# Kernel optimization log

Measured on AMD Instinct MI355X. Metric: run time of the kernel, lower is better.

Reference implementation:

```python
import jax, jax.numpy as jnp
import numpy as np

B, T, H, K = 4, 1024, 1024, 16
HD = H // K  # head dim
EPS = 1e-5


def _layernorm(x, g, b):
    mu = jnp.mean(x, axis=-1, keepdims=True)
    var = jnp.mean(jnp.square(x - mu), axis=-1, keepdims=True)
    return (x - mu) * jax.lax.rsqrt(var + EPS) * g + b


def setup_inputs() -> dict:
    key = jax.random.key(0)
    ks = jax.random.split(key, 16)
    s = 0.02
    return {
        "x": jax.random.normal(ks[0], (B, T, H), jnp.float32),
        "ln1_g": jnp.ones((H,), jnp.float32),
        "ln1_b": jnp.zeros((H,), jnp.float32),
        "ln2_g": jnp.ones((H,), jnp.float32),
        "ln2_b": jnp.zeros((H,), jnp.float32),
        "Wq": jax.random.normal(ks[1], (H, H), jnp.float32) * s,
        "bq": jnp.zeros((H,), jnp.float32),
        "Wk": jax.random.normal(ks[2], (H, H), jnp.float32) * s,
        "bk": jnp.zeros((H,), jnp.float32),
        "Wv": jax.random.normal(ks[3], (H, H), jnp.float32) * s,
        "bv": jnp.zeros((H,), jnp.float32),
        "W1": jax.random.normal(ks[4], (H, 4 * H), jnp.float32) * s,
        "b1": jnp.zeros((4 * H,), jnp.float32),
        "W2": jax.random.normal(ks[5], (4 * H, H), jnp.float32) * s,
        "b2": jnp.zeros((H,), jnp.float32),
    }


def reference(x, ln1_g, ln1_b, ln2_g, ln2_b, Wq, bq, Wk, bk, Wv, bv, W1, b1, W2, b2):
    # --- attention sub-block ---
    h = _layernorm(x, ln1_g, ln1_b)                      # (B,T,H)
    q = (h @ Wq + bq).reshape(B, T, K, HD).transpose(0, 2, 1, 3)  # (B,K,T,hd)
    k = (h @ Wk + bk).reshape(B, T, K, HD).transpose(0, 2, 1, 3)
    v = (h @ Wv + bv).reshape(B, T, K, HD).transpose(0, 2, 1, 3)
    qkt = jnp.einsum('bkqd,bkpd->bkqp', q, k)            # (B,K,T,T)
    attn = qkt * (1.0 / np.sqrt(HD))
    # module quirk: masked positions are FILLED with 1e-9 (not -inf) before softmax
    causal_mask = jnp.triu(jnp.ones((T, T), bool), k=1)  # True above diagonal = masked
    attn = jnp.where(causal_mask, jnp.float32(1e-9), attn)
    attn = jax.nn.softmax(attn, axis=-1)
    y = jnp.einsum('bkqp,bkpd->bkqd', attn, v)           # (B,K,T,hd)
    y = y.transpose(0, 2, 1, 3).reshape(B, T, H)
    x = x + y
    # --- MLP sub-block (dropout is identity at eval) ---
    h2 = _layernorm(x, ln2_g, ln2_b)
    m = jax.nn.gelu(h2 @ W1 + b1, approximate=False) @ W2 + b2
    return x + m
```

## Files before the change

### kernel.cpp

```cpp
#include <hip/hip_runtime.h>
#include <hip/hip_bf16.h>
#include <math.h>


typedef __attribute__((ext_vector_type(8))) short bf16x8;
typedef __attribute__((ext_vector_type(4))) float f32x4;

#define DEVINL __device__ __forceinline__

#define LOG2E_SCALE 0.18033688f
#define MASK2 1.4426950408889634e-9f

DEVINL void stage16(const __hip_bfloat16* g, short* l) {
  __builtin_amdgcn_global_load_lds(
      (const __attribute__((address_space(1))) unsigned int*)g,
      (__attribute__((address_space(3))) unsigned int*)l, 16, 0, 0);
}

DEVINL float bf2f(short u) {
  unsigned x = ((unsigned)(unsigned short)u) << 16;
  float f; __builtin_memcpy(&f, &x, 4); return f;
}

DEVINL short f2bf_s(float f) {
  __hip_bfloat16 h = __float2bfloat16(f);
  short s; __builtin_memcpy(&s, &h, 2); return s;
}

DEVINL float block_sum(float v, float* sb) {
  #pragma unroll
  for (int o = 32; o; o >>= 1) v += __shfl_down(v, o);
  const int lane = threadIdx.x & 63, w = threadIdx.x >> 6;
  if (lane == 0) sb[w] = v;
  __syncthreads();
  float r = sb[0] + sb[1] + sb[2] + sb[3];
  __syncthreads();
  return r;
}

template<int BM, int BN, int WM, int WN>
DEVINL void gemm_core64(const __hip_bfloat16* __restrict__ A, int lda,
                        const __hip_bfloat16* __restrict__ Bt, int ldb,
                        int Kd, int row0, int col0,
                        f32x4 (&acc)[WM/16][WN/16],
                        short* lds_a, short* lds_b) {
  constexpr int MI = WM / 16, NI = WN / 16, WNC = BN / WN;
  constexpr int CA = BM * 8, CB = BN * 8;
  const int tid = threadIdx.x;
  const int lane = tid & 63, wave = tid >> 6;
  const int wm = (wave / WNC) * WM, wn = (wave % WNC) * WN;
  const int lr = lane & 15, lq = lane >> 4;
  for (int k0 = 0; k0 < Kd; k0 += 64) {
    #pragma unroll
    for (int c = tid; c < CA; c += 256) {
      const int r = c >> 3, kc = ((c & 7) ^ (r & 7)) << 3;
      stage16(A + (size_t)(row0 + r) * lda + k0 + kc, lds_a + c * 8);
    }
    #pragma unroll
    for (int c = tid; c < CB; c += 256) {
      const int r = c >> 3, kc = ((c & 7) ^ (r & 7)) << 3;
      stage16(Bt + (size_t)(col0 + r) * ldb + k0 + kc, lds_b + c * 8);
    }
    __syncthreads();
    #pragma unroll
    for (int s = 0; s < 2; s++) {
      bf16x8 af[MI], bfr[NI];
      #pragma unroll
      for (int mi = 0; mi < MI; mi++) {
        const int m = wm + mi * 16 + lr;
        af[mi] = *(const bf16x8*)(lds_a + m * 64 + (((s * 4 + lq) ^ (m & 7)) << 3));
      }
      #pragma unroll
      for (int ni = 0; ni < NI; ni++) {
        const int n = wn + ni * 16 + lr;
        bfr[ni] = *(const bf16x8*)(lds_b + n * 64 + (((s * 4 + lq) ^ (n & 7)) << 3));
      }
      #pragma unroll
      for (int mi = 0; mi < MI; mi++)
        #pragma unroll
        for (int ni = 0; ni < NI; ni++)
          acc[mi][ni] = __builtin_amdgcn_mfma_f32_16x16x32_bf16(
              af[mi], bfr[ni], acc[mi][ni], 0, 0, 0);
    }
    __syncthreads();
  }
}

__global__ __launch_bounds__(256) void k_tcvt(const float* __restrict__ src,
                                              __hip_bfloat16* __restrict__ dst,
                                              int R, int C, int dstOff, int dstPitch) {
  __shared__ float tile[32][33];
  const int c0 = blockIdx.x * 32, r0 = blockIdx.y * 32;
  const int tx = threadIdx.x, ty = threadIdx.y;
  #pragma unroll
  for (int i = 0; i < 32; i += 8)
    tile[ty + i][tx] = src[(size_t)(r0 + ty + i) * C + c0 + tx];
  __syncthreads();
  #pragma unroll
  for (int i = 0; i < 32; i += 8)
    dst[(size_t)(c0 + ty + i + dstOff) * dstPitch + r0 + tx] =
        __float2bfloat16(tile[tx][ty + i]);
}

__global__ __launch_bounds__(256) void k_tcvt3(const float* __restrict__ Wq,
                                               const float* __restrict__ Wk,
                                               const float* __restrict__ Wv,
                                               __hip_bfloat16* __restrict__ dst) {
  __shared__ float tile[32][33];
  const float* src = blockIdx.z == 0 ? Wq : (blockIdx.z == 1 ? Wk : Wv);
  const int dstOff = blockIdx.z << 10;
  const int c0 = blockIdx.x * 32, r0 = blockIdx.y * 32;
  const int tx = threadIdx.x, ty = threadIdx.y;
  #pragma unroll
  for (int i = 0; i < 32; i += 8)
    tile[ty + i][tx] = src[(size_t)(r0 + ty + i) * 1024 + c0 + tx];
  __syncthreads();
  #pragma unroll
  for (int i = 0; i < 32; i += 8)
    dst[(size_t)(c0 + ty + i + dstOff) * 1024 + r0 + tx] =
        __float2bfloat16(tile[tx][ty + i]);
}

__global__ __launch_bounds__(256) void k_pack_bias(const float* __restrict__ bq,
                                                   const float* __restrict__ bk,
                                                   const float* __restrict__ bv,
                                                   float* __restrict__ o) {
  const int i = blockIdx.x * 256 + threadIdx.x;
  if (i < 3072)
    o[i] = i < 1024 ? bq[i] : (i < 2048 ? bk[i - 1024] : bv[i - 2048]);
}

__global__ __launch_bounds__(256) void k_ln(const float* __restrict__ x,
                                            const float* __restrict__ y,
                                            const float* __restrict__ g,
                                            const float* __restrict__ bb,
                                            __hip_bfloat16* __restrict__ o,
                                            const float* __restrict__ badd,
                                            float* __restrict__ oinit) {
  __shared__ float sb[4];
  const int t = threadIdx.x;
  const size_t base = (size_t)blockIdx.x * 1024 + t * 4;
  const int c = t * 4;
  float4 xv = *(const float4*)(x + base);
  if (y) {
    float4 yv = *(const float4*)(y + base);
    xv.x += yv.x; xv.y += yv.y; xv.z += yv.z; xv.w += yv.w;
    float4 ov;
    ov.x = xv.x + badd[c + 0]; ov.y = xv.y + badd[c + 1];
    ov.z = xv.z + badd[c + 2]; ov.w = xv.w + badd[c + 3];
    *(float4*)(oinit + base) = ov;
  }
  const float mu = block_sum(xv.x + xv.y + xv.z + xv.w, sb) * (1.f / 1024.f);
  const float dx = xv.x - mu, dy = xv.y - mu, dz = xv.z - mu, dw = xv.w - mu;
  const float var = block_sum(dx * dx + dy * dy + dz * dz + dw * dw, sb) * (1.f / 1024.f);
  const float rs = rsqrtf(var + 1e-5f);
  o[base + 0] = __float2bfloat16(dx * rs * g[c + 0] + bb[c + 0]);
  o[base + 1] = __float2bfloat16(dy * rs * g[c + 1] + bb[c + 1]);
  o[base + 2] = __float2bfloat16(dz * rs * g[c + 2] + bb[c + 2]);
  o[base + 3] = __float2bfloat16(dw * rs * g[c + 3] + bb[c + 3]);
}

__global__ __launch_bounds__(256) void k_gemm_qkv(
    const __hip_bfloat16* __restrict__ h1, const __hip_bfloat16* __restrict__ Wt,
    const float* __restrict__ bqkv, __hip_bfloat16* __restrict__ Q,
    __hip_bfloat16* __restrict__ K, __hip_bfloat16* __restrict__ Vt) {
  __shared__ alignas(16) short smem[16896];
  short* la = smem;
  short* lb = smem + 8192;
  short* lc = smem;
  const int row0 = blockIdx.x * 128, col0 = blockIdx.y * 128;
  f32x4 acc[4][4] = {};
  gemm_core64<128, 128, 64, 64>(h1, 1024, Wt, 1024, 1024, row0, col0, acc, la, lb);
  const int tid = threadIdx.x, lane = tid & 63, wave = tid >> 6;
  const int wm = (wave >> 1) * 64, wn = (wave & 1) * 64, lr = lane & 15, lq = lane >> 4;
  const int which = col0 >> 10;
  const int h0 = (col0 & 1023) >> 6;
  const int b = row0 >> 10, t0 = row0 & 1023;
  if (which < 2) {
    const float qs = (which == 0) ? LOG2E_SCALE : 1.f;
    #pragma unroll
    for (int mi = 0; mi < 4; mi++)
      #pragma unroll
      for (int ni = 0; ni < 4; ni++)
        #pragma unroll
        for (int r = 0; r < 4; r++) {
          const int row = wm + mi * 16 + lq * 4 + r;
          const int col = wn + ni * 16 + lr;
          lc[row * 132 + col] = f2bf_s((acc[mi][ni][r] + bqkv[col0 + col]) * qs);
        }
    __syncthreads();
    __hip_bfloat16* O = which == 0 ? Q : K;
    #pragma unroll
    for (int c = 0; c < 8; c++) {
      const int f = tid + 256 * c;
      const int r = f >> 4, cc = f & 15;
      const int col = cc * 8;
      const int head = h0 + (col >> 6), d = col & 63;
      float4 vv = *(const float4*)(lc + r * 132 + col);
      *(float4*)(O + (((size_t)(b * 16 + head)) << 16) + (t0 + r) * 64 + d) = vv;
    }
  } else {
    #pragma unroll
    for (int mi = 0; mi < 4; mi++)
      #pragma unroll
      for (int ni = 0; ni < 4; ni++)
        #pragma unroll
        for (int r = 0; r < 4; r++) {
          const int row = wm + mi * 16 + lq * 4 + r;
          const int col = wn + ni * 16 + lr;
          lc[col * 132 + row] = f2bf_s(acc[mi][ni][r] + bqkv[col0 + col]);
        }
    __syncthreads();
    #pragma unroll
    for (int c = 0; c < 8; c++) {
      const int f = tid + 256 * c;
      const int dl = f >> 4, tc = f & 15;
      const int head = h0 + (dl >> 6), d = dl & 63;
      float4 vv = *(const float4*)(lc + dl * 132 + tc * 8);
      *(float4*)(Vt + (((size_t)(b * 16 + head)) << 16) + (size_t)d * 1024 +
                 t0 + tc * 8) = vv;
    }
  }
}

__global__ __launch_bounds__(256) void k_tailv(const __hip_bfloat16* __restrict__ Vt,
                                               float* __restrict__ TV) {
  __shared__ float ts[8][64];
  const int hb = blockIdx.x, tid = threadIdx.x;
  const __hip_bfloat16* Vh = Vt + ((size_t)hb << 16);
  for (int w = tid; w < 512; w += 256) {
    const int kt = w >> 6, d = w & 63;
    const short* p = (const short*)(Vh + (size_t)d * 1024 + kt * 128);
    float s = 0.f;
    for (int j = 0; j < 128; j += 8) {
      bf16x8 v = *(const bf16x8*)(p + j);
      #pragma unroll
      for (int e = 0; e < 8; e++) s += bf2f(v[e]);
    }
    ts[kt][d] = s;
  }
  __syncthreads();
  for (int w = tid; w < 512; w += 256) {
    const int qt = w >> 6, d = w & 63;
    float s = 0.f;
    for (int kt = qt + 1; kt < 8; kt++) s += ts[kt][d];
    TV[((size_t)hb * 8 + qt) * 64 + d] = s;
  }
}

__global__ __launch_bounds__(256, 3) void k_attn(
    const __hip_bfloat16* __restrict__ Q, const __hip_bfloat16* __restrict__ K,
    const __hip_bfloat16* __restrict__ Vt, const float* __restrict__ TV,
    float* __restrict__ y) {
  __shared__ short lp[64 * 130];
  __shared__ short lK[128 * 64];
  __shared__ short lV[128 * 64];
  const int hb = blockIdx.y;
  const int j = (blockIdx.y & 32) ? (15 - (int)blockIdx.x) : (int)blockIdx.x;
  const int q0 = j * 64;
  const int nkt = (j >> 1) + 1;
  const int tid = threadIdx.x, lane = tid & 63, wave = tid >> 6;
  const int lr = lane & 15, lq = lane >> 4;
  const int wm = wave * 16;
  const __hip_bfloat16* Qh = Q + ((size_t)hb << 16);
  const __hip_bfloat16* Kh = K + ((size_t)hb << 16);
  const __hip_bfloat16* Vh = Vt + ((size_t)hb << 16);

  bf16x8 qf[2];
  #pragma unroll
  for (int s = 0; s < 2; s++)
    qf[s] = *(const bf16x8*)((const short*)Qh +
                             (size_t)(q0 + wm + lr) * 64 + s * 32 + lq * 8);

  f32x4 oacc[4] = {};
  float mrow[4], lrow[4];
  #pragma unroll
  for (int r = 0; r < 4; r++) { mrow[r] = -1e30f; lrow[r] = 0.f; }

  for (int c = tid; c < 1024; c += 256)
    stage16(Kh + (size_t)(c >> 3) * 64 + (((c & 7) ^ ((c >> 3) & 7)) << 3),
            lK + c * 8);
  __syncthreads();

  for (int kt = 0; kt < nkt; kt++) {
    const int k0 = kt * 128;
    f32x4 sacc[8] = {};
    __builtin_amdgcn_s_setprio(1);
    #pragma unroll
    for (int s = 0; s < 2; s++) {
      bf16x8 bf[8];
      #pragma unroll
      for (int ni = 0; ni < 8; ni++) {
        const int n = ni * 16 + lr;
        bf[ni] = *(const bf16x8*)(lK + n * 64 + (((s * 4 + lq) ^ (n & 7)) << 3));
      }
      #pragma unroll
      for (int ni = 0; ni < 8; ni++)
        sacc[ni] = __builtin_amdgcn_mfma_f32_16x16x32_bf16(
            qf[s], bf[ni], sacc[ni], 0, 0, 0);
    }
    __builtin_amdgcn_s_setprio(0);
    __syncthreads();
    for (int c = tid; c < 1024; c += 256)
      stage16(Vh + (size_t)(c >> 4) * 1024 + k0 + (((c & 15) ^ ((c >> 4) & 15)) << 3),
              lV + c * 8);
    if (kt + 1 < nkt) {
      const int k1 = k0 + 128;
      for (int c = tid; c < 1024; c += 256)
        stage16(Kh + (size_t)(k1 + (c >> 3)) * 64 + (((c & 7) ^ ((c >> 3) & 7)) << 3),
                lK + c * 8);
    }
    const bool last = (kt == nkt - 1);
    #pragma unroll
    for (int r = 0; r < 4; r++) {
      const int grow = q0 + wm + lq * 4 + r;
      float tmax = -1e30f;
      #pragma unroll
      for (int ni = 0; ni < 8; ni++) {
        float v = sacc[ni][r];
        if (last && (k0 + ni * 16 + lr) > grow) v = MASK2;
        sacc[ni][r] = v;
        tmax = fmaxf(tmax, v);
      }
      #pragma unroll
      for (int msk = 8; msk; msk >>= 1) tmax = fmaxf(tmax, __shfl_xor(tmax, msk));
      const float mn = fmaxf(mrow[r], tmax);
      const float al = __builtin_amdgcn_exp2f(mrow[r] - mn);
      float rs = 0.f;
      #pragma unroll
      for (int ni = 0; ni < 8; ni++) {
        const float pv = __builtin_amdgcn_exp2f(sacc[ni][r] - mn);
        sacc[ni][r] = pv;
        rs += pv;
      }
      #pragma unroll
      for (int msk = 8; msk; msk >>= 1) rs += __shfl_xor(rs, msk);
      mrow[r] = mn;
      lrow[r] = lrow[r] * al + rs;
      #pragma unroll
      for (int ni = 0; ni < 4; ni++) oacc[ni][r] *= al;
    }
    #pragma unroll
    for (int r = 0; r < 4; r++) {
      const int row = wm + lq * 4 + r;
      #pragma unroll
      for (int ni = 0; ni < 8; ni++)
        lp[row * 130 + ni * 16 + lr] = f2bf_s(sacc[ni][r]);
    }
    __syncthreads();
    __builtin_amdgcn_s_setprio(1);
    #pragma unroll
    for (int ks = 0; ks < 4; ks++) {
      bf16x8 pa, vb[4];
      pa = *(const bf16x8*)(lp + (wm + lr) * 130 + ks * 32 + lq * 8);
      #pragma unroll
      for (int ni = 0; ni < 4; ni++) {
        const int d = ni * 16 + lr;
        vb[ni] = *(const bf16x8*)(lV + d * 128 + (((ks * 4 + lq) ^ (d & 15)) << 3));
      }
      #pragma unroll
      for (int ni = 0; ni < 4; ni++)
        oacc[ni] = __builtin_amdgcn_mfma_f32_16x16x32_bf16(
            pa, vb[ni], oacc[ni], 0, 0, 0);
    }
    __builtin_amdgcn_s_setprio(0);
  }

  const int b = hb >> 4, h = hb & 15;
  const float cv = (float)(1024 - nkt * 128);
  const float* tv = TV + ((size_t)hb * 8 + (j >> 1)) * 64;
  #pragma unroll
  for (int r = 0; r < 4; r++) {
    const int t = q0 + wm + lq * 4 + r;
    const float tail = __builtin_amdgcn_exp2f(MASK2 - mrow[r]);
    const float inv = 1.f / (lrow[r] + cv * tail);
    #pragma unroll
    for (int ni = 0; ni < 4; ni++) {
      const int d = ni * 16 + lr;
      y[((size_t)(b * 1024 + t) << 10) + h * 64 + d] =
          (oacc[ni][r] + tail * tv[d]) * inv;
    }
  }
}

__global__ __launch_bounds__(256) void k_gemm_mlp1(const __hip_bfloat16* __restrict__ h2,
                                                   const __hip_bfloat16* __restrict__ W1t,
                                                   const float* __restrict__ b1,
                                                   __hip_bfloat16* __restrict__ G) {
  __shared__ alignas(16) short smem[16896];
  short* la = smem;
  short* lb = smem + 8192;
  short* lc = smem;
  const int row0 = blockIdx.x * 128, col0 = blockIdx.y * 128;
  f32x4 acc[4][4] = {};
  gemm_core64<128, 128, 64, 64>(h2, 1024, W1t, 1024, 1024, row0, col0, acc, la, lb);
  const int tid = threadIdx.x, lane = tid & 63, wave = tid >> 6;
  const int wm = (wave >> 1) * 64, wn = (wave & 1) * 64, lr = lane & 15, lq = lane >> 4;
  #pragma unroll
  for (int mi = 0; mi < 4; mi++)
    #pragma unroll
    for (int ni = 0; ni < 4; ni++)
      #pragma unroll
      for (int r = 0; r < 4; r++) {
        const int row = wm + mi * 16 + lq * 4 + r;
        const int col = wn + ni * 16 + lr;
        float v = acc[mi][ni][r] + b1[col0 + col];
        const float u = fminf(v * (2.3022079f + 0.1029434f * v * v), 80.f);
        const float e = __builtin_amdgcn_exp2f(u);
        v = v * e * __builtin_amdgcn_rcpf(e + 1.f);
        lc[row * 132 + col] = f2bf_s(v);
      }
  __syncthreads();
  #pragma unroll
  for (int c = 0; c < 8; c++) {
    const int f = tid + 256 * c;
    const int r = f >> 4, cc = f & 15;
    float4 vv = *(const float4*)(lc + r * 132 + cc * 8);
    *(float4*)(G + ((size_t)(row0 + r) << 12) + col0 + cc * 8) = vv;
  }
}

__global__ __launch_bounds__(256) void k_gemm_mlp2(const __hip_bfloat16* __restrict__ G,
                                                   const __hip_bfloat16* __restrict__ W2t,
                                                   float* __restrict__ out) {
  __shared__ alignas(16) short smem[12288];
  short* la = smem;
  short* lb = smem + 8192;
  const int row0 = blockIdx.x * 128, col0 = blockIdx.y * 64;
  const int kOff = blockIdx.z * 2048;
  f32x4 acc[4][2] = {};
  gemm_core64<128, 64, 64, 32>(G + kOff, 4096, W2t + kOff, 4096, 2048,
                               row0, col0, acc, la, lb);
  const int lane = threadIdx.x & 63, wave = threadIdx.x >> 6;
  const int wm = (wave >> 1) * 64, wn = (wave & 1) * 32, lr = lane & 15, lq = lane >> 4;
  #pragma unroll
  for (int mi = 0; mi < 4; mi++)
    #pragma unroll
    for (int ni = 0; ni < 2; ni++)
      #pragma unroll
      for (int r = 0; r < 4; r++) {
        const int grow = row0 + wm + mi * 16 + lq * 4 + r;
        const int gcol = col0 + wn + ni * 16 + lr;
        atomicAdd(out + (((size_t)grow << 10) + gcol), acc[mi][ni][r]);
      }
}

extern "C" void kernel_launch(void* const* d_in, const int* in_sizes, int n_in,
                              void* d_out, int out_size, void* d_ws, size_t ws_size,
                              hipStream_t stream) {
  const float* x     = (const float*)d_in[0];
  const float* ln1_g = (const float*)d_in[1];
  const float* ln1_b = (const float*)d_in[2];
  const float* ln2_g = (const float*)d_in[3];
  const float* ln2_b = (const float*)d_in[4];
  const float* Wq    = (const float*)d_in[5];
  const float* bq    = (const float*)d_in[6];
  const float* Wk    = (const float*)d_in[7];
  const float* bk    = (const float*)d_in[8];
  const float* Wv    = (const float*)d_in[9];
  const float* bv    = (const float*)d_in[10];
  const float* W1    = (const float*)d_in[11];
  const float* b1    = (const float*)d_in[12];
  const float* W2    = (const float*)d_in[13];
  const float* b2    = (const float*)d_in[14];
  float* out = (float*)d_out;

  char* p = (char*)d_ws;
  auto alloc = [&](size_t bytes) { char* r = p; p += (bytes + 255) & ~(size_t)255; return r; };
  __hip_bfloat16* wqkv = (__hip_bfloat16*)alloc(3072 * 1024 * 2);
  __hip_bfloat16* w1t  = (__hip_bfloat16*)alloc(4096 * 1024 * 2);
  __hip_bfloat16* w2t  = (__hip_bfloat16*)alloc(1024 * 4096 * 2);
  float*          bqkv = (float*)alloc(3072 * 4);
  __hip_bfloat16* h1   = (__hip_bfloat16*)alloc(4096 * 1024 * 2);
  __hip_bfloat16* Qb   = (__hip_bfloat16*)alloc((size_t)64 * 65536 * 2);
  __hip_bfloat16* Kb   = (__hip_bfloat16*)alloc((size_t)64 * 65536 * 2);
  __hip_bfloat16* Vt   = (__hip_bfloat16*)alloc((size_t)64 * 65536 * 2);
  float*          TV   = (float*)alloc((size_t)64 * 8 * 64 * 4);
  float*          yb   = (float*)alloc((size_t)4096 * 1024 * 4);
  __hip_bfloat16* h2   = (__hip_bfloat16*)alloc(4096 * 1024 * 2);
  __hip_bfloat16* G    = (__hip_bfloat16*)alloc((size_t)4096 * 4096 * 2);
  (void)ws_size; (void)in_sizes; (void)n_in; (void)out_size;

  const dim3 b256(256), bt(32, 8);
  k_tcvt3<<<dim3(32, 32, 3), bt, 0, stream>>>(Wq, Wk, Wv, wqkv);
  k_tcvt<<<dim3(128, 32), bt, 0, stream>>>(W1, w1t, 1024, 4096, 0, 1024);
  k_tcvt<<<dim3(32, 128), bt, 0, stream>>>(W2, w2t, 4096, 1024, 0, 4096);
  k_pack_bias<<<12, b256, 0, stream>>>(bq, bk, bv, bqkv);

  k_ln<<<4096, b256, 0, stream>>>(x, nullptr, ln1_g, ln1_b, h1, nullptr, nullptr);
  k_gemm_qkv<<<dim3(32, 24), b256, 0, stream>>>(h1, wqkv, bqkv, Qb, Kb, Vt);
  k_tailv<<<64, b256, 0, stream>>>(Vt, TV);
  k_attn<<<dim3(16, 64), b256, 0, stream>>>(Qb, Kb, Vt, TV, yb);

  k_ln<<<4096, b256, 0, stream>>>(x, yb, ln2_g, ln2_b, h2, b2, out);
  k_gemm_mlp1<<<dim3(32, 32), b256, 0, stream>>>(h2, w1t, b1, G);
  k_gemm_mlp2<<<dim3(32, 16, 2), b256, 0, stream>>>(G, w2t, out);
}
```

Before: 334.3 us.

## Rewrite MLP1 GEMM with 256x256 tiles, 512 threads, swizzled double-buffered LDS

Result: no change. 332.8 us (-0.4%).

```diff
diff --git a/kernel.cpp b/kernel.cpp
--- a/kernel.cpp
+++ b/kernel.cpp
@@ -383,40 +383,98 @@
   }
 }
 
-__global__ __launch_bounds__(256) void k_gemm_mlp1(const __hip_bfloat16* __restrict__ h2,
-                                                   const __hip_bfloat16* __restrict__ W1t,
-                                                   const float* __restrict__ b1,
-                                                   __hip_bfloat16* __restrict__ G) {
-  __shared__ alignas(16) short smem[16896];
-  short* la = smem;
-  short* lb = smem + 8192;
+__global__ __launch_bounds__(512, 2) void k_gemm_mlp1(const __hip_bfloat16* __restrict__ h2,
+                                                      const __hip_bfloat16* __restrict__ W1t,
+                                                      const float* __restrict__ b1,
+                                                      __hip_bfloat16* __restrict__ G) {
+  __shared__ alignas(16) short smem[32768];
+  const int row0 = blockIdx.x * 256, col0 = blockIdx.y * 256;
+  const int tid = threadIdx.x, lane = tid & 63, wid = tid >> 6;
+  const int lr = lane & 15, lq = lane >> 4;
+  const int wm = (wid >> 2) * 128, wn = (wid & 3) * 64;
+  const __hip_bfloat16* A = h2 + (size_t)row0 * 1024;
+  const __hip_bfloat16* Bt = W1t + (size_t)col0 * 1024;
+
+  auto STAGE = [&](const __hip_bfloat16* src, int k0, short* dst) {
+    #pragma unroll
+    for (int i = 0; i < 2; i++) {
+      const int f = tid + i * 512;
+      const int u = f >> 3, P = f & 7, Gc = P ^ (u & 7);
+      const int r = u * 2 + (Gc >> 2), g = Gc & 3;
+      stage16(src + (size_t)r * 1024 + k0 + g * 8, dst + f * 8);
+    }
+  };
+
+  f32x4 acc[8][4] = {};
+  STAGE(A, 0, smem);
+  STAGE(Bt, 0, smem + 16384);
+  for (int t = 0; t < 32; ++t) {
+    const int cur = t & 1;
+    short* pa = smem + cur * 8192;
+    short* pb = smem + 16384 + cur * 8192;
+    if (t + 1 < 32) {
+      short* na = smem + (cur ^ 1) * 8192;
+      short* nb = smem + 16384 + (cur ^ 1) * 8192;
+      STAGE(A, (t + 1) * 32, na);
+      STAGE(Bt, (t + 1) * 32, nb);
+      asm volatile("s_waitcnt vmcnt(4)" ::: "memory");
+    } else {
+      asm volatile("s_waitcnt vmcnt(0)" ::: "memory");
+    }
+    asm volatile("s_barrier" ::: "memory");
+    bf16x8 af[8], bfr[4];
+    #pragma unroll
+    for (int mi = 0; mi < 8; mi++) {
+      const int r = wm + mi * 16 + lr;
+      af[mi] = *(const bf16x8*)(pa + (r >> 1) * 64 +
+                ((((((r & 1) << 2) | lq)) ^ ((r >> 1) & 7)) << 3));
+    }
+    #pragma unroll
+    for (int ni = 0; ni < 4; ni++) {
+      const int n = wn + ni * 16 + lr;
+      bfr[ni] = *(const bf16x8*)(pb + (n >> 1) * 64 +
+                ((((((n & 1) << 2) | lq)) ^ ((n >> 1) & 7)) << 3));
+    }
+    __builtin_amdgcn_s_setprio(1);
+    #pragma unroll
+    for (int mi = 0; mi < 8; mi++)
+      #pragma unroll
+      for (int ni = 0; ni < 4; ni++)
+        acc[mi][ni] = __builtin_amdgcn_mfma_f32_16x16x32_bf16(
+            af[mi], bfr[ni], acc[mi][ni], 0, 0, 0);
+    __builtin_amdgcn_s_setprio(0);
+    asm volatile("s_barrier" ::: "memory");
+  }
+
   short* lc = smem;
-  const int row0 = blockIdx.x * 128, col0 = blockIdx.y * 128;
-  f32x4 acc[4][4] = {};
-  gemm_core64<128, 128, 64, 64>(h2, 1024, W1t, 1024, 1024, row0, col0, acc, la, lb);
-  const int tid = threadIdx.x, lane = tid & 63, wave = tid >> 6;
-  const int wm = (wave >> 1) * 64, wn = (wave & 1) * 64, lr = lane & 15, lq = lane >> 4;
-  #pragma unroll
-  for (int mi = 0; mi < 4; mi++)
-    #pragma unroll
-    for (int ni = 0; ni < 4; ni++)
-      #pragma unroll
-      for (int r = 0; r < 4; r++) {
-        const int row = wm + mi * 16 + lq * 4 + r;
-        const int col = wn + ni * 16 + lr;
-        float v = acc[mi][ni][r] + b1[col0 + col];
-        const float u = fminf(v * (2.3022079f + 0.1029434f * v * v), 80.f);
-        const float e = __builtin_amdgcn_exp2f(u);
-        v = v * e * __builtin_amdgcn_rcpf(e + 1.f);
-        lc[row * 132 + col] = f2bf_s(v);
-      }
-  __syncthreads();
-  #pragma unroll
-  for (int c = 0; c < 8; c++) {
-    const int f = tid + 256 * c;
-    const int r = f >> 4, cc = f & 15;
-    float4 vv = *(const float4*)(lc + r * 132 + cc * 8);
-    *(float4*)(G + ((size_t)(row0 + r) << 12) + col0 + cc * 8) = vv;
+  #pragma unroll
+  for (int pr = 0; pr < 4; pr++) {
+    if ((wid >> 2) == (pr >> 1)) {
+      const int mib = (pr & 1) * 4;
+      #pragma unroll
+      for (int mi2 = 0; mi2 < 4; mi2++)
+        #pragma unroll
+        for (int ni = 0; ni < 4; ni++)
+          #pragma unroll
+          for (int rr = 0; rr < 4; rr++) {
+            const int rloc = mi2 * 16 + lq * 4 + rr;
+            const int col = wn + ni * 16 + lr;
+            float v = acc[mib + mi2][ni][rr] + b1[col0 + col];
+            const float u2 = fminf(v * (2.3022079f + 0.1029434f * v * v), 80.f);
+            const float e = __builtin_amdgcn_exp2f(u2);
+            v = v * e * __builtin_amdgcn_rcpf(e + 1.f);
+            lc[rloc * 264 + col] = f2bf_s(v);
+          }
+    }
+    __syncthreads();
+    #pragma unroll
+    for (int c = 0; c < 4; c++) {
+      const int f = tid + 512 * c;
+      const int r = f >> 5, cc = f & 31;
+      float4 vv = *(const float4*)(lc + r * 264 + cc * 8);
+      *(float4*)(G + ((size_t)(row0 + pr * 64 + r) << 12) + col0 + cc * 8) = vv;
+    }
+    __syncthreads();
   }
 }
 
@@ -493,6 +551,6 @@
   k_attn<<<dim3(16, 64), b256, 0, stream>>>(Qb, Kb, Vt, TV, yb);
 
   k_ln<<<4096, b256, 0, stream>>>(x, yb, ln2_g, ln2_b, h2, b2, out);
-  k_gemm_mlp1<<<dim3(32, 32), b256, 0, stream>>>(h2, w1t, b1, G);
+  k_gemm_mlp1<<<dim3(16, 16), dim3(512), 0, stream>>>(h2, w1t, b1, G);
   k_gemm_mlp2<<<dim3(32, 16, 2), b256, 0, stream>>>(G, w2t, out);
 }
```
